# Performance work log

Hardware: AMD Instinct MI355X
Metric: run time of the kernel (lower is better)

Reference implementation:

```python
import jax, jax.numpy as jnp
import numpy as np

RADIUS = [3, 3, 4, 4]
DILATION = [1, 2, 1, 2]
N_HEAD = 4
D_K = 8
SCALE = 1.0 / np.sqrt(8.0)  # module hardcodes sqrt(8)


def _patches(a, r, d):
    # a: (b, t, c, h, w) -> (b, t, c, ls2, h, w), dilated (2r+1)x(2r+1) window,
    # zero padding (invalid positions masked separately).
    b, t, c, h, w = a.shape
    p = r * d
    ap = jnp.pad(a, ((0, 0), (0, 0), (0, 0), (p, p), (p, p)))
    ls = 2 * r + 1
    sl = [ap[..., dy * d:dy * d + h, dx * d:dx * d + w]
          for dy in range(ls) for dx in range(ls)]
    return jnp.stack(sl, axis=3)


def _valid_mask(h, w, r, d):
    # (ls2, h, w) bool: True where window position is inside the image
    m = _patches(jnp.ones((1, 1, 1, h, w)), r, d)
    return m[0, 0, 0] > 0.5


def _head_attn(q, k, v, r, d):
    # q,k,v: (b, t, c, h, w); attention over all t' frames x local window
    b, t, c, h, w = q.shape
    kp = _patches(k, r, d)        # (b, t', c, p, h, w)
    vp = _patches(v, r, d)
    valid = _valid_mask(h, w, r, d)  # (p, h, w)
    e = jnp.einsum('btchw,bscphw->btsphw', q, kp) * SCALE
    e = jnp.where(valid[None, None, None], e, -jnp.inf)  # OOB -> -inf like CUDA kernel
    e = e.reshape(b, t, t * valid.shape[0], h, w)
    attn = jax.nn.softmax(e, axis=2).reshape(b, t, t, -1, h, w)
    return jnp.einsum('btsphw,bscphw->btchw', attn, vp)


def setup_inputs() -> dict:
    key = jax.random.key(0)
    kx, kq, kk, kv, ko = jax.random.split(key, 5)
    C = 32
    std = 1.0 / np.sqrt(C)
    x = jax.random.normal(kx, (2, 5, C, 64, 64), dtype=jnp.float32)
    Wq = jax.random.normal(kq, (N_HEAD * D_K, C), dtype=jnp.float32) * std
    Wk = jax.random.normal(kk, (N_HEAD * D_K, C), dtype=jnp.float32) * std
    Wv = jax.random.normal(kv, (N_HEAD * D_K, C), dtype=jnp.float32) * std
    Wo = jax.random.normal(ko, (C, C), dtype=jnp.float32) * std
    return {"x": x, "Wq": Wq, "Wk": Wk, "Wv": Wv, "Wo": Wo}


def reference(x, Wq, Wk, Wv, Wo):
    # 1x1x1 Conv3d == per-pixel channel matmul
    q = jnp.einsum('btchw,kc->btkhw', x, Wq)
    k = jnp.einsum('btchw,kc->btkhw', x, Wk)
    v = jnp.einsum('btchw,kc->btkhw', x, Wv)
    outs = []
    for i in range(N_HEAD):
        s = slice(i * D_K, (i + 1) * D_K)
        outs.append(_head_attn(q[:, :, s], k[:, :, s], v[:, :, s],
                               RADIUS[i], DILATION[i]))
    out = jnp.concatenate(outs, axis=2)
    out = jnp.einsum('btchw,kc->btkhw', out, Wo)
    return out + x
```

## Files before the change

### kernel.cpp

```cpp
#include <hip/hip_runtime.h>
#include <stdint.h>

#define NT 5
#define NC 32
#define NH 4
#define HW 4096
#define NPIX 40960
#define QS 0.51006972789f
#define EBIAS 12.0f

typedef _Float16 half_t;
typedef half_t h2 __attribute__((ext_vector_type(2)));

static __device__ __forceinline__ h2 as_h2(uint32_t u) {
  union { uint32_t u; h2 h; } c; c.u = u; return c.h;
}
static __device__ __forceinline__ uint32_t pack_h2(float a, float b) {
  union { h2 h; uint32_t u; } c;
  c.h.x = (half_t)a; c.h.y = (half_t)b;
  return c.u;
}

#if __has_builtin(__builtin_amdgcn_exp2f)
#define EXP2(x) __builtin_amdgcn_exp2f(x)
#else
#define EXP2(x) exp2f(x)
#endif

static __device__ __forceinline__ float dot8b(const uint4& a, const uint4& b) {
#if __has_builtin(__builtin_amdgcn_fdot2)
  float c = -EBIAS;
  c = __builtin_amdgcn_fdot2(as_h2(a.x), as_h2(b.x), c, false);
  c = __builtin_amdgcn_fdot2(as_h2(a.y), as_h2(b.y), c, false);
  c = __builtin_amdgcn_fdot2(as_h2(a.z), as_h2(b.z), c, false);
  c = __builtin_amdgcn_fdot2(as_h2(a.w), as_h2(b.w), c, false);
  return c;
#else
  const h2 a0 = as_h2(a.x), a1 = as_h2(a.y), a2 = as_h2(a.z), a3 = as_h2(a.w);
  const h2 b0 = as_h2(b.x), b1 = as_h2(b.y), b2 = as_h2(b.z), b3 = as_h2(b.w);
  float c = -EBIAS;
  c = fmaf((float)a0.x, (float)b0.x, c);
  c = fmaf((float)a0.y, (float)b0.y, c);
  c = fmaf((float)a1.x, (float)b1.x, c);
  c = fmaf((float)a1.y, (float)b1.y, c);
  c = fmaf((float)a2.x, (float)b2.x, c);
  c = fmaf((float)a2.y, (float)b2.y, c);
  c = fmaf((float)a3.x, (float)b3.x, c);
  c = fmaf((float)a3.y, (float)b3.y, c);
  return c;
#endif
}

__global__ __launch_bounds__(256) void qkv_kernel(
    const float* __restrict__ x,
    const float* __restrict__ Wq, const float* __restrict__ Wk,
    const float* __restrict__ Wv,
    uint4* __restrict__ qf, uint4* __restrict__ kf, uint4* __restrict__ vf,
    float* __restrict__ accbuf)
{
  const int p   = blockIdx.x * 256 + threadIdx.x;
  const int h   = blockIdx.y;
  const int bt  = p >> 12;
  const int pix = p & 4095;

  const int gid = (blockIdx.y * 160 + blockIdx.x) * 256 + threadIdx.x;
  #pragma unroll
  for (int i = 0; i < 9; ++i) accbuf[(size_t)i * 163840 + gid] = 0.f;

  const float* xp = x + (size_t)bt * (NC * HW) + pix;
  float xc[NC];
  #pragma unroll
  for (int c = 0; c < NC; ++c) xc[c] = xp[(size_t)c * HW];

  float qv[8], kv8[8], vv8[8];
  #pragma unroll
  for (int j = 0; j < 8; ++j) {
    const int o = h * 8 + j;
    float aq = 0.f, ak = 0.f, av = 0.f;
    #pragma unroll
    for (int c = 0; c < NC; ++c) {
      const float xv = xc[c];
      aq = fmaf(xv, Wq[o * NC + c], aq);
      ak = fmaf(xv, Wk[o * NC + c], ak);
      av = fmaf(xv, Wv[o * NC + c], av);
    }
    qv[j] = aq * QS; kv8[j] = ak; vv8[j] = av;
  }
  const size_t base = ((size_t)bt * NH + h) * HW + pix;
  uint4 qq, kk, vv;
  qq.x = pack_h2(qv[0], qv[1]);  qq.y = pack_h2(qv[2], qv[3]);
  qq.z = pack_h2(qv[4], qv[5]);  qq.w = pack_h2(qv[6], qv[7]);
  kk.x = pack_h2(kv8[0], kv8[1]); kk.y = pack_h2(kv8[2], kv8[3]);
  kk.z = pack_h2(kv8[4], kv8[5]); kk.w = pack_h2(kv8[6], kv8[7]);
  vv.x = pack_h2(vv8[0], vv8[1]); vv.y = pack_h2(vv8[2], vv8[3]);
  vv.z = pack_h2(vv8[4], vv8[5]); vv.w = pack_h2(vv8[6], vv8[7]);
  qf[base] = qq;
  kf[base] = kk;
  vf[base] = vv;
}

template <int R, int D>
static __device__ __forceinline__ void attn_body(
    int b, int t, int h, int s, int yb,
    const uint4* __restrict__ qf, const uint4* __restrict__ kf,
    const uint4* __restrict__ vf, float* __restrict__ accbuf,
    uint4* __restrict__ k_lds, uint4* __restrict__ v_lds)
{
  constexpr int LS    = 2 * R + 1;
  constexpr int NROWS = 8 + 2 * R;
  const int tid  = threadIdx.x;
  const int w    = tid >> 6;
  const int lane = tid & 63;

  const int y0 = (D == 1) ? (yb * 8) : ((yb & 1) + 2 * ((yb >> 1) * 8));

  const uint4* kg = kf + (size_t)((b * NT + s) * NH + h) * HW;
  const uint4* vg = vf + (size_t)((b * NT + s) * NH + h) * HW;
  for (int idx = tid; idx < NROWS * 64; idx += 256) {
    const int r  = idx >> 6, xs = idx & 63;
    int ys = y0 + (r - R) * D;
    ys = ys < 0 ? 0 : (ys > 63 ? 63 : ys);
    const int pos = (D == 1) ? xs : ((xs & 1) * 32 + (xs >> 1));
    k_lds[r * 64 + pos] = kg[ys * 64 + xs];
    v_lds[r * 64 + pos] = vg[ys * 64 + xs];
  }
  __syncthreads();

  const int xp = lane >> 5;
  const int cb = (D == 1) ? lane : (lane & 31);
  const int x  = (D == 1) ? lane : (2 * (lane & 31) + xp);
  const int yA = y0 + 2 * w * D;
  const int yB = yA + D;
  const int pixA = yA * 64 + x, pixB = yB * 64 + x;

  const uint4* qp = qf + (size_t)((b * NT + t) * NH + h) * HW;
  const uint4 qA = qp[pixA];
  const uint4 qB = qp[pixB];

  float lA = 0.f, lB = 0.f;
  h2 aA[4], aB[4];
  const h2 z2 = { (half_t)0.f, (half_t)0.f };
  #pragma unroll
  for (int i = 0; i < 4; ++i) { aA[i] = z2; aB[i] = z2; }

  #pragma unroll 1
  for (int u = 0; u <= LS; ++u) {
    const bool okA = (u < LS) && ((unsigned)(yA + (u - R) * D) < 64u);
    const bool okB = (u > 0)  && ((unsigned)(yB + (u - 1 - R) * D) < 64u);
    if (!(okA || okB)) continue;
    const float mA = okA ? 1.f : 0.f, mB = okB ? 1.f : 0.f;
    const uint4* kr = k_lds + (2 * w + u) * 64;
    const uint4* vr = v_lds + (2 * w + u) * 64;
    #pragma unroll
    for (int dx = -R; dx <= R; ++dx) {
      const int  cx  = cb + dx;
      const bool okx = (unsigned)cx < (D == 1 ? 64u : 32u);
      const int  cc  = okx ? cx : 0;
      const int  pos = (D == 1) ? cc : (xp * 32 + cc);
      const uint4 kk = kr[pos];
      const uint4 vv = vr[pos];
      const h2 w0 = as_h2(vv.x), w1 = as_h2(vv.y), w2 = as_h2(vv.z), w3 = as_h2(vv.w);
      const float eA = dot8b(qA, kk);
      const float eB = dot8b(qB, kk);
      const float pA = (okx ? mA : 0.f) * EXP2(eA);
      const float pB = (okx ? mB : 0.f) * EXP2(eB);
      lA += pA; lB += pB;
      const half_t pAh = (half_t)pA, pBh = (half_t)pB;
      const h2 pA2 = { pAh, pAh }, pB2 = { pBh, pBh };
      aA[0] += pA2 * w0; aA[1] += pA2 * w1; aA[2] += pA2 * w2; aA[3] += pA2 * w3;
      aB[0] += pB2 * w0; aB[1] += pB2 * w1; aB[2] += pB2 * w2; aB[3] += pB2 * w3;
    }
  }

  const int btA = (b * NT + t) * HW + pixA;
  const int btB = (b * NT + t) * HW + pixB;
  float* ab = accbuf + (size_t)(h * 9) * NPIX;
  #pragma unroll
  for (int i = 0; i < 4; ++i) {
    atomicAdd(&ab[(size_t)(2 * i)     * NPIX + btA], (float)aA[i].x);
    atomicAdd(&ab[(size_t)(2 * i + 1) * NPIX + btA], (float)aA[i].y);
    atomicAdd(&ab[(size_t)(2 * i)     * NPIX + btB], (float)aB[i].x);
    atomicAdd(&ab[(size_t)(2 * i + 1) * NPIX + btB], (float)aB[i].y);
  }
  atomicAdd(&ab[(size_t)8 * NPIX + btA], lA);
  atomicAdd(&ab[(size_t)8 * NPIX + btB], lB);
}

__global__ __launch_bounds__(256) void attn_kernel(
    const uint4* __restrict__ qf, const uint4* __restrict__ kf,
    const uint4* __restrict__ vf, float* __restrict__ accbuf)
{
  __shared__ uint4 k_lds[16 * 64];
  __shared__ uint4 v_lds[16 * 64];
  const int bid = blockIdx.x;
  const int h   = bid & 3;
  int r = bid >> 2;
  const int yb = r & 7; r >>= 3;
  const int s  = r % 5;
  const int bt = r / 5;
  const int t = bt % NT, b = bt / NT;
  if      (h == 0) attn_body<3, 1>(b, t, 0, s, yb, qf, kf, vf, accbuf, k_lds, v_lds);
  else if (h == 1) attn_body<3, 2>(b, t, 1, s, yb, qf, kf, vf, accbuf, k_lds, v_lds);
  else if (h == 2) attn_body<4, 1>(b, t, 2, s, yb, qf, kf, vf, accbuf, k_lds, v_lds);
  else             attn_body<4, 2>(b, t, 3, s, yb, qf, kf, vf, accbuf, k_lds, v_lds);
}

__global__ __launch_bounds__(64) void proj_kernel(
    const float* __restrict__ accbuf, const float* __restrict__ x,
    const float* __restrict__ Wo, float* __restrict__ out)
{
  const int p   = blockIdx.x * 64 + threadIdx.x;
  const int bt  = p >> 12;
  const int pix = p & 4095;

  float oc[32];
  #pragma unroll
  for (int h = 0; h < NH; ++h) {
    const float* ab = accbuf + (size_t)(h * 9) * NPIX + p;
    float a[8];
    #pragma unroll
    for (int i = 0; i < 8; ++i) a[i] = ab[(size_t)i * NPIX];
    const float inv = 1.0f / ab[(size_t)8 * NPIX];
    #pragma unroll
    for (int i = 0; i < 8; ++i) oc[h * 8 + i] = a[i] * inv;
  }

  const float* xp = x + (size_t)bt * (NC * HW) + pix;
  float* yp = out + (size_t)bt * (NC * HW) + pix;
  #pragma unroll
  for (int o = 0; o < NC; ++o) {
    float acc = xp[(size_t)o * HW];
    #pragma unroll
    for (int c = 0; c < NC; ++c)
      acc = fmaf(oc[c], Wo[o * NC + c], acc);
    yp[(size_t)o * HW] = acc;
  }
}

extern "C" void kernel_launch(void* const* d_in, const int* in_sizes, int n_in,
                              void* d_out, int out_size, void* d_ws, size_t ws_size,
                              hipStream_t stream)
{
  const float* x  = (const float*)d_in[0];
  const float* Wq = (const float*)d_in[1];
  const float* Wk = (const float*)d_in[2];
  const float* Wv = (const float*)d_in[3];
  const float* Wo = (const float*)d_in[4];

  char* ws = (char*)d_ws;
  uint4* qf  = (uint4*)ws;
  uint4* kf  = (uint4*)(ws + 2621440);
  uint4* vf  = (uint4*)(ws + 2 * 2621440);
  float* acc = (float*)(ws + 3 * 2621440);

  qkv_kernel<<<dim3(160, 4), 256, 0, stream>>>(x, Wq, Wk, Wv, qf, kf, vf, acc);
  attn_kernel<<<1600, 256, 0, stream>>>(qf, kf, vf, acc);
  proj_kernel<<<640, 64, 0, stream>>>(acc, x, Wo, (float*)d_out);
}
```

Measured before the change: 132.3 us.

## Compute four query rows per wave to reuse each K/V LDS load

Each wave now handles four output rows instead of two. Every K/V entry read from LDS is reused across four queries, and validity masking is folded into the dot-product bias as -inf. Blocks shrink to 128 threads while tile coverage per block stays the same, so there are fewer LDS reads per FLOP but half the threads per block. The cost is higher register pressure from the four query rows and 4x4 accumulators, plus lower parallelism per block.

```diff
diff --git a/kernel.cpp b/kernel.cpp
--- a/kernel.cpp
+++ b/kernel.cpp
@@ -8,6 +8,7 @@
 #define NPIX 40960
 #define QS 0.51006972789f
 #define EBIAS 12.0f
+#define NINF (-__builtin_inff())
 
 typedef _Float16 half_t;
 typedef half_t h2 __attribute__((ext_vector_type(2)));
@@ -27,9 +28,8 @@
 #define EXP2(x) exp2f(x)
 #endif
 
-static __device__ __forceinline__ float dot8b(const uint4& a, const uint4& b) {
+static __device__ __forceinline__ float dot8i(const uint4& a, const uint4& b, float c) {
 #if __has_builtin(__builtin_amdgcn_fdot2)
-  float c = -EBIAS;
   c = __builtin_amdgcn_fdot2(as_h2(a.x), as_h2(b.x), c, false);
   c = __builtin_amdgcn_fdot2(as_h2(a.y), as_h2(b.y), c, false);
   c = __builtin_amdgcn_fdot2(as_h2(a.z), as_h2(b.z), c, false);
@@ -38,7 +38,6 @@
 #else
   const h2 a0 = as_h2(a.x), a1 = as_h2(a.y), a2 = as_h2(a.z), a3 = as_h2(a.w);
   const h2 b0 = as_h2(b.x), b1 = as_h2(b.y), b2 = as_h2(b.z), b3 = as_h2(b.w);
-  float c = -EBIAS;
   c = fmaf((float)a0.x, (float)b0.x, c);
   c = fmaf((float)a0.y, (float)b0.y, c);
   c = fmaf((float)a1.x, (float)b1.x, c);
@@ -106,87 +105,99 @@
     const uint4* __restrict__ vf, float* __restrict__ accbuf,
     uint4* __restrict__ k_lds, uint4* __restrict__ v_lds)
 {
-  constexpr int LS    = 2 * R + 1;
   constexpr int NROWS = 8 + 2 * R;
+  constexpr int CMAX  = (D == 1) ? 64 : 32;
   const int tid  = threadIdx.x;
   const int w    = tid >> 6;
   const int lane = tid & 63;
 
-  const int y0 = (D == 1) ? (yb * 8) : ((yb & 1) + 2 * ((yb >> 1) * 8));
+  const int y0c    = (D == 1) ? (yb * 8) : ((yb >> 1) * 8);
+  const int parity = (D == 1) ? 0 : (yb & 1);
 
   const uint4* kg = kf + (size_t)((b * NT + s) * NH + h) * HW;
   const uint4* vg = vf + (size_t)((b * NT + s) * NH + h) * HW;
-  for (int idx = tid; idx < NROWS * 64; idx += 256) {
+  for (int idx = tid; idx < NROWS * 64; idx += 128) {
     const int r  = idx >> 6, xs = idx & 63;
-    int ys = y0 + (r - R) * D;
-    ys = ys < 0 ? 0 : (ys > 63 ? 63 : ys);
+    int yc = y0c + r - R;
+    yc = yc < 0 ? 0 : (yc > CMAX - 1 ? CMAX - 1 : yc);
+    const int ys  = (D == 1) ? yc : (parity + 2 * yc);
     const int pos = (D == 1) ? xs : ((xs & 1) * 32 + (xs >> 1));
     k_lds[r * 64 + pos] = kg[ys * 64 + xs];
     v_lds[r * 64 + pos] = vg[ys * 64 + xs];
   }
   __syncthreads();
 
-  const int xp = lane >> 5;
-  const int cb = (D == 1) ? lane : (lane & 31);
-  const int x  = (D == 1) ? lane : (2 * (lane & 31) + xp);
-  const int yA = y0 + 2 * w * D;
-  const int yB = yA + D;
-  const int pixA = yA * 64 + x, pixB = yB * 64 + x;
-
+  const int xpar = lane >> 5;
+  const int cb   = (D == 1) ? lane : (lane & 31);
+  const int x    = (D == 1) ? lane : (2 * (lane & 31) + xpar);
+
+  int ypix[4];
   const uint4* qp = qf + (size_t)((b * NT + t) * NH + h) * HW;
-  const uint4 qA = qp[pixA];
-  const uint4 qB = qp[pixB];
-
-  float lA = 0.f, lB = 0.f;
-  h2 aA[4], aB[4];
+  uint4 q[4];
+  #pragma unroll
+  for (int i = 0; i < 4; ++i) {
+    const int yc = y0c + w * 4 + i;
+    const int y  = (D == 1) ? yc : (parity + 2 * yc);
+    ypix[i] = y * 64 + x;
+    q[i] = qp[ypix[i]];
+  }
+
+  float l[4] = {0.f, 0.f, 0.f, 0.f};
+  h2 a[4][4];
   const h2 z2 = { (half_t)0.f, (half_t)0.f };
   #pragma unroll
-  for (int i = 0; i < 4; ++i) { aA[i] = z2; aB[i] = z2; }
+  for (int i = 0; i < 4; ++i)
+    #pragma unroll
+    for (int j = 0; j < 4; ++j) a[i][j] = z2;
 
   #pragma unroll 1
-  for (int u = 0; u <= LS; ++u) {
-    const bool okA = (u < LS) && ((unsigned)(yA + (u - R) * D) < 64u);
-    const bool okB = (u > 0)  && ((unsigned)(yB + (u - 1 - R) * D) < 64u);
-    if (!(okA || okB)) continue;
-    const float mA = okA ? 1.f : 0.f, mB = okB ? 1.f : 0.f;
-    const uint4* kr = k_lds + (2 * w + u) * 64;
-    const uint4* vr = v_lds + (2 * w + u) * 64;
+  for (int u = 0; u < 2 * R + 4; ++u) {
+    const int kyc = y0c + w * 4 + u - R;
+    if ((unsigned)kyc >= (unsigned)CMAX) continue;
+    float bi[4];
+    #pragma unroll
+    for (int i = 0; i < 4; ++i)
+      bi[i] = (u >= i && u <= i + 2 * R) ? -EBIAS : NINF;
+    const uint4* kr = k_lds + (w * 4 + u) * 64;
+    const uint4* vr = v_lds + (w * 4 + u) * 64;
     #pragma unroll
     for (int dx = -R; dx <= R; ++dx) {
       const int  cx  = cb + dx;
-      const bool okx = (unsigned)cx < (D == 1 ? 64u : 32u);
+      const bool okx = (unsigned)cx < (unsigned)CMAX;
       const int  cc  = okx ? cx : 0;
-      const int  pos = (D == 1) ? cc : (xp * 32 + cc);
+      const int  pos = (D == 1) ? cc : (xpar * 32 + cc);
       const uint4 kk = kr[pos];
       const uint4 vv = vr[pos];
       const h2 w0 = as_h2(vv.x), w1 = as_h2(vv.y), w2 = as_h2(vv.z), w3 = as_h2(vv.w);
-      const float eA = dot8b(qA, kk);
-      const float eB = dot8b(qB, kk);
-      const float pA = (okx ? mA : 0.f) * EXP2(eA);
-      const float pB = (okx ? mB : 0.f) * EXP2(eB);
-      lA += pA; lB += pB;
-      const half_t pAh = (half_t)pA, pBh = (half_t)pB;
-      const h2 pA2 = { pAh, pAh }, pB2 = { pBh, pBh };
-      aA[0] += pA2 * w0; aA[1] += pA2 * w1; aA[2] += pA2 * w2; aA[3] += pA2 * w3;
-      aB[0] += pB2 * w0; aB[1] += pB2 * w1; aB[2] += pB2 * w2; aB[3] += pB2 * w3;
+      const float eo = okx ? 0.f : NINF;
+      #pragma unroll
+      for (int i = 0; i < 4; ++i) {
+        const float e = dot8i(q[i], kk, bi[i] + eo);
+        const float p = EXP2(e);
+        l[i] += p;
+        const half_t ph = (half_t)p;
+        const h2 p2 = { ph, ph };
+        a[i][0] += p2 * w0; a[i][1] += p2 * w1;
+        a[i][2] += p2 * w2; a[i][3] += p2 * w3;
+      }
     }
   }
 
-  const int btA = (b * NT + t) * HW + pixA;
-  const int btB = (b * NT + t) * HW + pixB;
+  const int btbase = (b * NT + t) * HW;
   float* ab = accbuf + (size_t)(h * 9) * NPIX;
   #pragma unroll
   for (int i = 0; i < 4; ++i) {
-    atomicAdd(&ab[(size_t)(2 * i)     * NPIX + btA], (float)aA[i].x);
-    atomicAdd(&ab[(size_t)(2 * i + 1) * NPIX + btA], (float)aA[i].y);
-    atomicAdd(&ab[(size_t)(2 * i)     * NPIX + btB], (float)aB[i].x);
-    atomicAdd(&ab[(size_t)(2 * i + 1) * NPIX + btB], (float)aB[i].y);
-  }
-  atomicAdd(&ab[(size_t)8 * NPIX + btA], lA);
-  atomicAdd(&ab[(size_t)8 * NPIX + btB], lB);
-}
-
-__global__ __launch_bounds__(256) void attn_kernel(
+    const int bp = btbase + ypix[i];
+    #pragma unroll
+    for (int j = 0; j < 4; ++j) {
+      atomicAdd(&ab[(size_t)(2 * j)     * NPIX + bp], (float)a[i][j].x);
+      atomicAdd(&ab[(size_t)(2 * j + 1) * NPIX + bp], (float)a[i][j].y);
+    }
+    atomicAdd(&ab[(size_t)8 * NPIX + bp], l[i]);
+  }
+}
+
+__global__ __launch_bounds__(128) void attn_kernel(
     const uint4* __restrict__ qf, const uint4* __restrict__ kf,
     const uint4* __restrict__ vf, float* __restrict__ accbuf)
 {
@@ -254,6 +265,6 @@
   float* acc = (float*)(ws + 3 * 2621440);
 
   qkv_kernel<<<dim3(160, 4), 256, 0, stream>>>(x, Wq, Wk, Wv, qf, kf, vf, acc);
-  attn_kernel<<<1600, 256, 0, stream>>>(qf, kf, vf, acc);
+  attn_kernel<<<1600, 128, 0, stream>>>(qf, kf, vf, acc);
   proj_kernel<<<640, 64, 0, stream>>>(acc, x, Wo, (float*)d_out);
 }
```

After: 151.1 us. 14.2% more time.

## Replace atomic accumulation with per-source-frame partial buffers reduced in projection

Applied to the files above, without the earlier changes.

Each attention block now writes its partial numerator (packed fp16) and denominator for its source frame into a dedicated plane, instead of issuing float atomicAdds into a shared accumulator. The projection kernel sums the five source-frame partials before normalising, and the accumulator zeroing in the QKV kernel is removed. This is meant to remove atomic contention and the zero-fill traffic. In exchange the workspace grows and the partial sums are stored in fp16, which may cost some precision.

```diff
diff --git a/kernel.cpp b/kernel.cpp
--- a/kernel.cpp
+++ b/kernel.cpp
@@ -55,17 +55,12 @@
     const float* __restrict__ x,
     const float* __restrict__ Wq, const float* __restrict__ Wk,
     const float* __restrict__ Wv,
-    uint4* __restrict__ qf, uint4* __restrict__ kf, uint4* __restrict__ vf,
-    float* __restrict__ accbuf)
+    uint4* __restrict__ qf, uint4* __restrict__ kf, uint4* __restrict__ vf)
 {
   const int p   = blockIdx.x * 256 + threadIdx.x;
   const int h   = blockIdx.y;
   const int bt  = p >> 12;
   const int pix = p & 4095;
-
-  const int gid = (blockIdx.y * 160 + blockIdx.x) * 256 + threadIdx.x;
-  #pragma unroll
-  for (int i = 0; i < 9; ++i) accbuf[(size_t)i * 163840 + gid] = 0.f;
 
   const float* xp = x + (size_t)bt * (NC * HW) + pix;
   float xc[NC];
@@ -103,7 +98,8 @@
 static __device__ __forceinline__ void attn_body(
     int b, int t, int h, int s, int yb,
     const uint4* __restrict__ qf, const uint4* __restrict__ kf,
-    const uint4* __restrict__ vf, float* __restrict__ accbuf,
+    const uint4* __restrict__ vf,
+    uint4* __restrict__ pa, float* __restrict__ pl,
     uint4* __restrict__ k_lds, uint4* __restrict__ v_lds)
 {
   constexpr int LS    = 2 * R + 1;
@@ -172,23 +168,19 @@
     }
   }
 
-  const int btA = (b * NT + t) * HW + pixA;
-  const int btB = (b * NT + t) * HW + pixB;
-  float* ab = accbuf + (size_t)(h * 9) * NPIX;
-  #pragma unroll
-  for (int i = 0; i < 4; ++i) {
-    atomicAdd(&ab[(size_t)(2 * i)     * NPIX + btA], (float)aA[i].x);
-    atomicAdd(&ab[(size_t)(2 * i + 1) * NPIX + btA], (float)aA[i].y);
-    atomicAdd(&ab[(size_t)(2 * i)     * NPIX + btB], (float)aB[i].x);
-    atomicAdd(&ab[(size_t)(2 * i + 1) * NPIX + btB], (float)aB[i].y);
-  }
-  atomicAdd(&ab[(size_t)8 * NPIX + btA], lA);
-  atomicAdd(&ab[(size_t)8 * NPIX + btB], lB);
+  const size_t plane = (size_t)(s * NH + h) * NPIX + (size_t)(b * NT + t) * HW;
+  union { h2 hh[4]; uint4 u; } cA, cB;
+  #pragma unroll
+  for (int i = 0; i < 4; ++i) { cA.hh[i] = aA[i]; cB.hh[i] = aB[i]; }
+  pa[plane + pixA] = cA.u;
+  pa[plane + pixB] = cB.u;
+  pl[plane + pixA] = lA;
+  pl[plane + pixB] = lB;
 }
 
 __global__ __launch_bounds__(256) void attn_kernel(
     const uint4* __restrict__ qf, const uint4* __restrict__ kf,
-    const uint4* __restrict__ vf, float* __restrict__ accbuf)
+    const uint4* __restrict__ vf, uint4* __restrict__ pa, float* __restrict__ pl)
 {
   __shared__ uint4 k_lds[16 * 64];
   __shared__ uint4 v_lds[16 * 64];
@@ -199,15 +191,16 @@
   const int s  = r % 5;
   const int bt = r / 5;
   const int t = bt % NT, b = bt / NT;
-  if      (h == 0) attn_body<3, 1>(b, t, 0, s, yb, qf, kf, vf, accbuf, k_lds, v_lds);
-  else if (h == 1) attn_body<3, 2>(b, t, 1, s, yb, qf, kf, vf, accbuf, k_lds, v_lds);
-  else if (h == 2) attn_body<4, 1>(b, t, 2, s, yb, qf, kf, vf, accbuf, k_lds, v_lds);
-  else             attn_body<4, 2>(b, t, 3, s, yb, qf, kf, vf, accbuf, k_lds, v_lds);
+  if      (h == 0) attn_body<3, 1>(b, t, 0, s, yb, qf, kf, vf, pa, pl, k_lds, v_lds);
+  else if (h == 1) attn_body<3, 2>(b, t, 1, s, yb, qf, kf, vf, pa, pl, k_lds, v_lds);
+  else if (h == 2) attn_body<4, 1>(b, t, 2, s, yb, qf, kf, vf, pa, pl, k_lds, v_lds);
+  else             attn_body<4, 2>(b, t, 3, s, yb, qf, kf, vf, pa, pl, k_lds, v_lds);
 }
 
 __global__ __launch_bounds__(64) void proj_kernel(
-    const float* __restrict__ accbuf, const float* __restrict__ x,
-    const float* __restrict__ Wo, float* __restrict__ out)
+    const uint4* __restrict__ pa, const float* __restrict__ pl,
+    const float* __restrict__ x, const float* __restrict__ Wo,
+    float* __restrict__ out)
 {
   const int p   = blockIdx.x * 64 + threadIdx.x;
   const int bt  = p >> 12;
@@ -216,11 +209,21 @@
   float oc[32];
   #pragma unroll
   for (int h = 0; h < NH; ++h) {
-    const float* ab = accbuf + (size_t)(h * 9) * NPIX + p;
-    float a[8];
-    #pragma unroll
-    for (int i = 0; i < 8; ++i) a[i] = ab[(size_t)i * NPIX];
-    const float inv = 1.0f / ab[(size_t)8 * NPIX];
+    float a[8], l = 0.f;
+    #pragma unroll
+    for (int i = 0; i < 8; ++i) a[i] = 0.f;
+    #pragma unroll
+    for (int s = 0; s < NT; ++s) {
+      const size_t plane = (size_t)(s * NH + h) * NPIX + p;
+      const uint4 v = pa[plane];
+      l += pl[plane];
+      const h2 v0 = as_h2(v.x), v1 = as_h2(v.y), v2 = as_h2(v.z), v3 = as_h2(v.w);
+      a[0] += (float)v0.x; a[1] += (float)v0.y;
+      a[2] += (float)v1.x; a[3] += (float)v1.y;
+      a[4] += (float)v2.x; a[5] += (float)v2.y;
+      a[6] += (float)v3.x; a[7] += (float)v3.y;
+    }
+    const float inv = 1.0f / l;
     #pragma unroll
     for (int i = 0; i < 8; ++i) oc[h * 8 + i] = a[i] * inv;
   }
@@ -248,12 +251,13 @@
   const float* Wo = (const float*)d_in[4];
 
   char* ws = (char*)d_ws;
-  uint4* qf  = (uint4*)ws;
-  uint4* kf  = (uint4*)(ws + 2621440);
-  uint4* vf  = (uint4*)(ws + 2 * 2621440);
-  float* acc = (float*)(ws + 3 * 2621440);
-
-  qkv_kernel<<<dim3(160, 4), 256, 0, stream>>>(x, Wq, Wk, Wv, qf, kf, vf, acc);
-  attn_kernel<<<1600, 256, 0, stream>>>(qf, kf, vf, acc);
-  proj_kernel<<<640, 64, 0, stream>>>(acc, x, Wo, (float*)d_out);
-}
+  uint4* qf = (uint4*)ws;
+  uint4* kf = (uint4*)(ws + 2621440);
+  uint4* vf = (uint4*)(ws + 2 * 2621440);
+  uint4* pa = (uint4*)(ws + 3 * 2621440);
+  float* pl = (float*)(ws + 3 * 2621440 + 13107200);
+
+  qkv_kernel<<<dim3(160, 4), 256, 0, stream>>>(x, Wq, Wk, Wv, qf, kf, vf);
+  attn_kernel<<<1600, 256, 0, stream>>>(qf, kf, vf, pa, pl);
+  proj_kernel<<<640, 64, 0, stream>>>(pa, pl, x, Wo, (float*)d_out);
+}
```

Measured after the change: 133.3 us. Within noise of the previous version (+0.8%).
